# Performance work log

Measured on AMD Instinct MI355X. Metric: run time of the kernel, lower is better.

Reference implementation:

```python
import jax, jax.numpy as jnp
import numpy as np

EPS = 1e-6
THRESHOLD = 0.99
MAX_STEPS = 4
MIN_STEPS = 1
N_HEAD = 8
B, N, D, V, L, F, RCF = 1, 256, 512, 32000, 2, 1536, 2048


def rmsnorm(x, w):
    return x * jax.lax.rsqrt(jnp.mean(x * x, axis=-1, keepdims=True) + EPS) * w


def rope(x, base=10000.0):
    # x: [B, N, H, hd] -> rotary embedding (rotate-half convention)
    n, hd = x.shape[1], x.shape[-1]
    half = hd // 2
    inv = 1.0 / (base ** (jnp.arange(half, dtype=jnp.float32) * 2.0 / hd))
    ang = jnp.arange(n, dtype=jnp.float32)[:, None] * inv[None, :]  # [N, half]
    cos = jnp.cos(ang)[None, :, None, :]
    sin = jnp.sin(ang)[None, :, None, :]
    x1, x2 = x[..., :half], x[..., half:]
    return jnp.concatenate([x1 * cos - x2 * sin, x1 * sin + x2 * cos], axis=-1)


def attention(x, wqkv, wo):
    b, n, d = x.shape
    hd = d // N_HEAD
    q, k, v = jnp.split(x @ wqkv, 3, axis=-1)
    q = rope(q.reshape(b, n, N_HEAD, hd))
    k = rope(k.reshape(b, n, N_HEAD, hd))
    v = v.reshape(b, n, N_HEAD, hd)
    scores = jnp.einsum('bqhd,bkhd->bhqk', q, k) / np.float32(np.sqrt(hd))
    causal = jnp.tril(jnp.ones((n, n), dtype=bool))
    scores = jnp.where(causal, scores, jnp.float32(-1e30))
    a = jax.nn.softmax(scores, axis=-1)
    out = jnp.einsum('bhqk,bkhd->bqhd', a, v).reshape(b, n, d)
    return out @ wo


def backbone(input_ids, emb, attn_norm_w, mlp_norm_w, wqkv, wo, w_gate, w_up, w_down, final_norm_w):
    x = emb[input_ids]  # [B, N, D]
    for l in range(L):  # small fixed layer count
        x = x + attention(rmsnorm(x, attn_norm_w[l]), wqkv[l], wo[l])
        h = rmsnorm(x, mlp_norm_w[l])
        x = x + (jax.nn.silu(h @ w_gate[l]) * (h @ w_up[l])) @ w_down[l]  # SwiGLU
    return rmsnorm(x, final_norm_w)


def refinement_step(states, rc_norm_w, rc_w1, rc_w2, w_y, w_delta, w_halt, b_halt):
    h = rmsnorm(states, rc_norm_w)
    y_logits = h @ w_y                                   # [B, N, V]
    refined = states + jax.nn.gelu(h @ rc_w1) @ rc_w2    # [B, N, D]
    delta_logits = rmsnorm(refined, rc_norm_w) @ w_delta # [B, N, V]
    halt = jax.nn.sigmoid(h @ w_halt + b_halt)           # [B, N]
    combined = y_logits + delta_logits                   # compute_prediction
    return combined, halt, refined


def act_combine(halt_probs, step_logits):
    # Vectorized version of the per-(b,n) ACT halting loop.
    # halt_probs: [B, N, S]; step_logits: [B, N, S, V]
    p = halt_probs.at[..., :MIN_STEPS].set(0.0)  # min-step masking (max_steps > min_steps)
    cum = jnp.cumsum(p, axis=-1)
    prev = cum - p                      # exclusive cumulative halting prob
    running = prev < THRESHOLD          # step still executes
    is_last = jnp.arange(p.shape[-1]) == p.shape[-1] - 1
    use_rem = running & ((cum >= THRESHOLD) | is_last)  # halting step gets remainder
    weights = jnp.where(running, jnp.where(use_rem, 1.0 - prev, p), 0.0)
    final = jnp.einsum('bns,bnsv->bnv', weights, step_logits)
    remainder = jnp.sum(jnp.where(use_rem, 1.0 - prev, 0.0), axis=-1)
    ponder = jnp.sum(running, axis=-1).astype(p.dtype) + remainder  # N + R ponder cost
    return final, ponder, weights


def reference(input_ids, emb, attn_norm_w, mlp_norm_w, wqkv, wo, w_gate, w_up, w_down,
              final_norm_w, rc_norm_w, rc_w1, rc_w2, w_y, w_delta, w_halt, b_halt):
    hidden = backbone(input_ids, emb, attn_norm_w, mlp_norm_w, wqkv, wo,
                      w_gate, w_up, w_down, final_norm_w)
    states = hidden
    logits_steps, halt_steps = [], []
    for _ in range(MAX_STEPS):  # fixed refinement unroll
        combined, halt, states = refinement_step(states, rc_norm_w, rc_w1, rc_w2,
                                                 w_y, w_delta, w_halt, b_halt)
        logits_steps.append(combined)
        halt_steps.append(halt)
    step_logits = jnp.stack(logits_steps, axis=2)  # [B, N, S, V]
    halt_probs = jnp.stack(halt_steps, axis=2)     # [B, N, S]
    final_logits, ponder_costs, all_weights = act_combine(halt_probs, step_logits)
    return final_logits, ponder_costs, all_weights


def setup_inputs() -> dict:
    key = jax.random.key(0)
    ks = jax.random.split(key, 16)
    s = 0.02
    return {
        'input_ids': jax.random.randint(ks[0], (B, N), 0, V),
        'emb': jax.random.normal(ks[1], (V, D), jnp.float32) * s,
        'attn_norm_w': jnp.ones((L, D), jnp.float32),
        'mlp_norm_w': jnp.ones((L, D), jnp.float32),
        'wqkv': jax.random.normal(ks[2], (L, D, 3 * D), jnp.float32) * s,
        'wo': jax.random.normal(ks[3], (L, D, D), jnp.float32) * s,
        'w_gate': jax.random.normal(ks[4], (L, D, F), jnp.float32) * s,
        'w_up': jax.random.normal(ks[5], (L, D, F), jnp.float32) * s,
        'w_down': jax.random.normal(ks[6], (L, F, D), jnp.float32) * s,
        'final_norm_w': jnp.ones((D,), jnp.float32),
        'rc_norm_w': jnp.ones((D,), jnp.float32),
        'rc_w1': jax.random.normal(ks[7], (D, RCF), jnp.float32) * s,
        'rc_w2': jax.random.normal(ks[8], (RCF, D), jnp.float32) * s,
        'w_y': jax.random.normal(ks[9], (D, V), jnp.float32) * s,
        'w_delta': jax.random.normal(ks[10], (D, V), jnp.float32) * s,
        'w_halt': jax.random.normal(ks[11], (D,), jnp.float32) * s,
        'b_halt': jnp.zeros((), jnp.float32),
    }
```

## Files before the change

kernel.cpp:

```cpp
#include <hip/hip_runtime.h>
#include <hip/hip_bf16.h>

#define NTOK   256
#define DMODEL 512
#define NHEAD  8
#define HD     64
#define HALF   32
#define FF     1536
#define RCFF   2048
#define VOCAB  32000
#define NLAYER 2
#define NSTEPS 4
#define EPSV   1e-6f
#define THR    0.99f

typedef __attribute__((ext_vector_type(8))) short bf16x8;
typedef __attribute__((ext_vector_type(4))) float f32x4;

__global__ __launch_bounds__(256) void k_embed_norm(const int* __restrict__ ids,
                                                    const float* __restrict__ emb,
                                                    const float* __restrict__ w,
                                                    float* __restrict__ x,
                                                    float* __restrict__ xn) {
    int row = blockIdx.x, t = threadIdx.x;
    int id = ids[row];
    const float* er = emb + (size_t)id * DMODEL;
    float v0 = er[t], v1 = er[t + 256];
    float ss = v0 * v0 + v1 * v1;
    __shared__ float red[4];
    int lane = t & 63, wv = t >> 6;
    for (int o = 32; o > 0; o >>= 1) ss += __shfl_xor(ss, o);
    if (lane == 0) red[wv] = ss;
    __syncthreads();
    float tot = red[0] + red[1] + red[2] + red[3];
    float scale = rsqrtf(tot * (1.f / DMODEL) + EPSV);
    size_t base = (size_t)row * DMODEL;
    x[base + t] = v0;
    x[base + t + 256] = v1;
    xn[base + t] = v0 * scale * w[t];
    xn[base + t + 256] = v1 * scale * w[t + 256];
}

__global__ __launch_bounds__(256) void k_rmsnorm(const float* __restrict__ in,
                                                 const float* __restrict__ w,
                                                 float* __restrict__ out) {
    int row = blockIdx.x;
    const float* xr = in + (size_t)row * DMODEL;
    float s = 0.f;
    for (int d = threadIdx.x; d < DMODEL; d += 256) { float v = xr[d]; s += v * v; }
    __shared__ float red[4];
    int lane = threadIdx.x & 63, wv = threadIdx.x >> 6;
    for (int o = 32; o > 0; o >>= 1) s += __shfl_xor(s, o);
    if (lane == 0) red[wv] = s;
    __syncthreads();
    float tot = red[0] + red[1] + red[2] + red[3];
    float scale = rsqrtf(tot * (1.f / DMODEL) + EPSV);
    for (int d = threadIdx.x; d < DMODEL; d += 256)
        out[(size_t)row * DMODEL + d] = xr[d] * scale * w[d];
}

__global__ __launch_bounds__(256) void k_mm_part(const float* __restrict__ A,
                                                 const float* __restrict__ W,
                                                 float* __restrict__ Cp,
                                                 int K, int N, int kc) {
    __shared__ float As[16][68];
    __shared__ float Ws[16][68];
    const int bn = blockIdx.x * 64;
    const int bm = blockIdx.y * 64;
    const int kz = blockIdx.z * kc;
    const int tx = threadIdx.x & 15;
    const int ty = threadIdx.x >> 4;
    float ar[4], wr[4];
#pragma unroll
    for (int r = 0; r < 4; ++r) {
        int idx = threadIdx.x + r * 256;
        int m = idx >> 4, kk = idx & 15;
        ar[r] = A[(size_t)(bm + m) * K + kz + kk];
        int n = idx & 63, kw = idx >> 6;
        wr[r] = W[(size_t)(kz + kw) * N + bn + n];
    }
    float acc[4][4] = {};
    for (int k0 = kz; k0 < kz + kc; k0 += 16) {
#pragma unroll
        for (int r = 0; r < 4; ++r) {
            int idx = threadIdx.x + r * 256;
            int m = idx >> 4, kk = idx & 15;
            As[kk][m] = ar[r];
            int n = idx & 63, kw = idx >> 6;
            Ws[kw][n] = wr[r];
        }
        __syncthreads();
        if (k0 + 16 < kz + kc) {
#pragma unroll
            for (int r = 0; r < 4; ++r) {
                int idx = threadIdx.x + r * 256;
                int m = idx >> 4, kk = idx & 15;
                ar[r] = A[(size_t)(bm + m) * K + k0 + 16 + kk];
                int n = idx & 63, kw = idx >> 6;
                wr[r] = W[(size_t)(k0 + 16 + kw) * N + bn + n];
            }
        }
#pragma unroll
        for (int kk = 0; kk < 16; ++kk) {
            float4 av = *(const float4*)&As[kk][ty * 4];
            float4 bv = *(const float4*)&Ws[kk][tx * 4];
            float a[4] = {av.x, av.y, av.z, av.w};
            float b[4] = {bv.x, bv.y, bv.z, bv.w};
#pragma unroll
            for (int i = 0; i < 4; ++i)
#pragma unroll
                for (int j = 0; j < 4; ++j)
                    acc[i][j] = fmaf(a[i], b[j], acc[i][j]);
        }
        __syncthreads();
    }
    float* cp = Cp + (size_t)blockIdx.z * (size_t)(gridDim.y * 64) * N;
#pragma unroll
    for (int i = 0; i < 4; ++i) {
        int m = bm + ty * 4 + i;
#pragma unroll
        for (int j = 0; j < 4; ++j)
            cp[(size_t)m * N + bn + tx * 4 + j] = acc[i][j];
    }
}

__global__ __launch_bounds__(256) void k_gu_part(const float* __restrict__ A,
                                                 const float* __restrict__ Wg,
                                                 const float* __restrict__ Wu,
                                                 float* __restrict__ GU) {
    __shared__ float As[16][68];
    __shared__ float Ws[16][68];
    const int bn = blockIdx.x * 64;
    const int bm = blockIdx.y * 64;
    const int z = blockIdx.z;
    const float* W = (z >> 1) ? Wu : Wg;
    const int kz = (z & 1) * 256;
    const int tx = threadIdx.x & 15;
    const int ty = threadIdx.x >> 4;
    float ar[4], wr[4];
#pragma unroll
    for (int r = 0; r < 4; ++r) {
        int idx = threadIdx.x + r * 256;
        int m = idx >> 4, kk = idx & 15;
        ar[r] = A[(size_t)(bm + m) * DMODEL + kz + kk];
        int n = idx & 63, kw = idx >> 6;
        wr[r] = W[(size_t)(kz + kw) * FF + bn + n];
    }
    float acc[4][4] = {};
    for (int k0 = kz; k0 < kz + 256; k0 += 16) {
#pragma unroll
        for (int r = 0; r < 4; ++r) {
            int idx = threadIdx.x + r * 256;
            int m = idx >> 4, kk = idx & 15;
            As[kk][m] = ar[r];
            int n = idx & 63, kw = idx >> 6;
            Ws[kw][n] = wr[r];
        }
        __syncthreads();
        if (k0 + 16 < kz + 256) {
#pragma unroll
            for (int r = 0; r < 4; ++r) {
                int idx = threadIdx.x + r * 256;
                int m = idx >> 4, kk = idx & 15;
                ar[r] = A[(size_t)(bm + m) * DMODEL + k0 + 16 + kk];
                int n = idx & 63, kw = idx >> 6;
                wr[r] = W[(size_t)(k0 + 16 + kw) * FF + bn + n];
            }
        }
#pragma unroll
        for (int kk = 0; kk < 16; ++kk) {
            float4 av = *(const float4*)&As[kk][ty * 4];
            float4 bv = *(const float4*)&Ws[kk][tx * 4];
            float a[4] = {av.x, av.y, av.z, av.w};
            float b[4] = {bv.x, bv.y, bv.z, bv.w};
#pragma unroll
            for (int i = 0; i < 4; ++i)
#pragma unroll
                for (int j = 0; j < 4; ++j)
                    acc[i][j] = fmaf(a[i], b[j], acc[i][j]);
        }
        __syncthreads();
    }
    float* cp = GU + (size_t)z * (NTOK * FF);
#pragma unroll
    for (int i = 0; i < 4; ++i) {
        int m = bm + ty * 4 + i;
#pragma unroll
        for (int j = 0; j < 4; ++j)
            cp[(size_t)m * FF + bn + tx * 4 + j] = acc[i][j];
    }
}

__global__ void k_mm_finish(const float* __restrict__ Cp, const float* __restrict__ res,
                            float* __restrict__ C, int tot, int zstride, int nz, int act) {
    int i = blockIdx.x * 256 + threadIdx.x;
    if (i >= tot) return;
    float s = 0.f;
    for (int z = 0; z < nz; ++z) s += Cp[(size_t)z * zstride + i];
    if (res) s += res[i];
    if (act == 1) {
        float xg = s;
        float inner = 0.79788456080286536f * (xg + 0.044715f * xg * xg * xg);
        s = 0.5f * xg * (1.f + tanhf(inner));
    }
    C[i] = s;
}

__global__ void k_finish_silumul(const float* __restrict__ GU, float* __restrict__ C) {
    int i = blockIdx.x * 256 + threadIdx.x;
    float g = GU[i] + GU[(size_t)(NTOK * FF) + i];
    float u = GU[(size_t)(2 * NTOK * FF) + i] + GU[(size_t)(3 * NTOK * FF) + i];
    float sig = 1.f / (1.f + expf(-g));
    C[i] = g * sig * u;
}

__global__ __launch_bounds__(256) void k_finish_norm(const float* __restrict__ Cp,
                                                     const float* __restrict__ res,
                                                     const float* __restrict__ normw,
                                                     float* __restrict__ out_raw,
                                                     float* __restrict__ out_norm,
                                                     int nz) {
    int row = blockIdx.x, t = threadIdx.x;
    int c0 = t, c1 = t + 256;
    size_t base = (size_t)row * DMODEL;
    float v0 = 0.f, v1 = 0.f;
    for (int z = 0; z < nz; ++z) {
        size_t zb = (size_t)z * (NTOK * DMODEL) + base;
        v0 += Cp[zb + c0];
        v1 += Cp[zb + c1];
    }
    v0 += res[base + c0];
    v1 += res[base + c1];
    float ss = v0 * v0 + v1 * v1;
    __shared__ float red[4];
    int lane = t & 63, wv = t >> 6;
    for (int o = 32; o > 0; o >>= 1) ss += __shfl_xor(ss, o);
    if (lane == 0) red[wv] = ss;
    __syncthreads();
    float tot = red[0] + red[1] + red[2] + red[3];
    float scale = rsqrtf(tot * (1.f / DMODEL) + EPSV);
    out_raw[base + c0] = v0;
    out_raw[base + c1] = v1;
    out_norm[base + c0] = v0 * scale * normw[c0];
    out_norm[base + c1] = v1 * scale * normw[c1];
}

__global__ __launch_bounds__(256) void k_qkv_finish_rope(const float* __restrict__ Cp,
                                                         float* __restrict__ qkv) {
    int pos = blockIdx.x, t = threadIdx.x;
    int h = t >> 5, d = t & 31;
    size_t base = (size_t)pos * FF;
    auto S = [&](int col) {
        float s = 0.f;
#pragma unroll
        for (int z = 0; z < 4; ++z) s += Cp[(size_t)z * (NTOK * FF) + base + col];
        return s;
    };
    int cq0 = h * HD + d, cq1 = cq0 + HALF;
    int ck0 = DMODEL + cq0, ck1 = ck0 + HALF;
    int cv0 = 2 * DMODEL + t, cv1 = cv0 + 256;
    float q0 = S(cq0), q1 = S(cq1);
    float k0 = S(ck0), k1 = S(ck1);
    float v0 = S(cv0), v1 = S(cv1);
    float inv = powf(10000.f, -(float)d / 32.f);
    float ang = (float)pos * inv;
    float c = cosf(ang), s = sinf(ang);
    qkv[base + cq0] = q0 * c - q1 * s;
    qkv[base + cq1] = q0 * s + q1 * c;
    qkv[base + ck0] = k0 * c - k1 * s;
    qkv[base + ck1] = k0 * s + k1 * c;
    qkv[base + cv0] = v0;
    qkv[base + cv1] = v1;
}

__global__ __launch_bounds__(256) void k_attn(const float* __restrict__ qkv,
                                              float* __restrict__ out) {
    int h = blockIdx.x;
    int qi = blockIdx.y;
    int t = threadIdx.x;
    __shared__ float qs[HD];
    __shared__ float ps[NTOK];
    __shared__ float red[4];
    __shared__ float red2[4];
    __shared__ float os[4][HD];
    if (t < HD) qs[t] = qkv[(size_t)qi * FF + h * HD + t];
    __syncthreads();
    float sc = -1e30f;
    if (t <= qi) {
        const float* kr = qkv + (size_t)t * FF + DMODEL + h * HD;
        float s = 0.f;
        for (int d = 0; d < HD; ++d) s = fmaf(qs[d], kr[d], s);
        sc = s * 0.125f;
    }
    float m = sc;
    for (int o = 32; o > 0; o >>= 1) m = fmaxf(m, __shfl_xor(m, o));
    int lane = t & 63, wv = t >> 6;
    if (lane == 0) red[wv] = m;
    __syncthreads();
    m = fmaxf(fmaxf(red[0], red[1]), fmaxf(red[2], red[3]));
    float e = (t <= qi) ? expf(sc - m) : 0.f;
    ps[t] = e;
    float sum = e;
    for (int o = 32; o > 0; o >>= 1) sum += __shfl_xor(sum, o);
    if (lane == 0) red2[wv] = sum;
    __syncthreads();
    sum = red2[0] + red2[1] + red2[2] + red2[3];
    float inv = 1.f / sum;
    int d = t & 63, g = t >> 6;
    float acc = 0.f;
    for (int ki = g; ki <= qi; ki += 4)
        acc = fmaf(ps[ki], qkv[(size_t)ki * FF + 2 * DMODEL + h * HD + d], acc);
    os[g][d] = acc * inv;
    __syncthreads();
    if (t < HD)
        out[(size_t)qi * DMODEL + h * HD + t] = os[0][t] + os[1][t] + os[2][t] + os[3][t];
}

__global__ __launch_bounds__(256) void k_haltactab(const float* __restrict__ H,
                                                   const float* __restrict__ wh,
                                                   const float* __restrict__ bptr,
                                                   float* __restrict__ ponder_out,
                                                   float* __restrict__ w_out,
                                                   __hip_bfloat16* __restrict__ A,
                                                   __hip_bfloat16* __restrict__ Bm) {
    int i = blockIdx.x, t = threadIdx.x;
    int lane = t & 63, wv = t >> 6;
    __shared__ float red[4];
    __shared__ float hvals[3];
    __shared__ float hw[4];
    for (int s = 1; s <= 3; ++s) {
        const float* hr = H + ((size_t)s * NTOK + i) * DMODEL;
        float a = hr[t] * wh[t] + hr[t + 256] * wh[t + 256];
        for (int o = 32; o > 0; o >>= 1) a += __shfl_xor(a, o);
        if (lane == 0) red[wv] = a;
        __syncthreads();
        if (t == 0)
            hvals[s - 1] = 1.f / (1.f + expf(-(red[0] + red[1] + red[2] + red[3] + bptr[0])));
        __syncthreads();
    }
    if (t == 0) {
        float p[4] = {0.f, hvals[0], hvals[1], hvals[2]};
        float cum = 0.f, rem = 0.f;
        int nrun = 0;
#pragma unroll
        for (int s = 0; s < 4; ++s) {
            float prev = cum;
            cum += p[s];
            bool running = prev < THR;
            bool use_rem = running && ((cum >= THR) || (s == 3));
            float v = 0.f;
            if (running) {
                v = use_rem ? (1.f - prev) : p[s];
                if (use_rem) rem += (1.f - prev);
                nrun++;
            }
            hw[s] = v;
            w_out[i * 4 + s] = v;
        }
        ponder_out[i] = (float)nrun + rem;
    }
    __syncthreads();
    float w0 = hw[0], w1 = hw[1], w2 = hw[2], w3 = hw[3];
    size_t base = (size_t)i * DMODEL;
#pragma unroll
    for (int r = 0; r < 2; ++r) {
        int d = t + r * 256;
        float h0 = H[base + d];
        float h1 = H[(size_t)(NTOK * DMODEL) + base + d];
        float h2 = H[(size_t)(2 * NTOK * DMODEL) + base + d];
        float h3 = H[(size_t)(3 * NTOK * DMODEL) + base + d];
        float h4 = H[(size_t)(4 * NTOK * DMODEL) + base + d];
        A[base + d]  = __float2bfloat16(w0 * h0 + w1 * h1 + w2 * h2 + w3 * h3);
        Bm[base + d] = __float2bfloat16(w0 * h1 + w1 * h2 + w2 * h3 + w3 * h4);
    }
}

__global__ __launch_bounds__(512) void k_logits_mfma(const __hip_bfloat16* __restrict__ Abf,
                                                     const __hip_bfloat16* __restrict__ Bbf,
                                                     const float* __restrict__ Wy,
                                                     const float* __restrict__ Wd,
                                                     float* __restrict__ out) {
    __shared__ short Alds[256 * 32];
    __shared__ short Blds[256 * 32];
    __shared__ short Wys[32 * 70];
    __shared__ short Wds[32 * 70];
    const int tid  = threadIdx.x;
    const int wave = tid >> 6;
    const int lane = tid & 63;
    const int wrow = (wave & 1) * 128;
    const int wcol = (wave >> 1) * 16;
    const int cl   = lane & 15;
    const int kg   = lane >> 4;
    const int col  = blockIdx.x * 64 + wcol + cl;

    const int kr = tid >> 4;
    const int c4 = (tid & 15) * 4;
    const int sr0 = tid >> 2;
    const int skp = (tid & 3) * 8;

    f32x4 acc[8];
#pragma unroll
    for (int i = 0; i < 8; ++i) acc[i] = (f32x4){0.f, 0.f, 0.f, 0.f};

    const float* gy = Wy + (size_t)kr * VOCAB + blockIdx.x * 64 + c4;
    const float* gd = Wd + (size_t)kr * VOCAB + blockIdx.x * 64 + c4;

    float4 ry = *(const float4*)gy;
    float4 rd = *(const float4*)gd;
    bf16x8 ra0 = *(const bf16x8*)(Abf + (size_t)sr0 * DMODEL + skp);
    bf16x8 ra1 = *(const bf16x8*)(Abf + (size_t)(sr0 + 128) * DMODEL + skp);
    bf16x8 rb0 = *(const bf16x8*)(Bbf + (size_t)sr0 * DMODEL + skp);
    bf16x8 rb1 = *(const bf16x8*)(Bbf + (size_t)(sr0 + 128) * DMODEL + skp);

    for (int t = 0; t < 16; ++t) {
        __syncthreads();
        {
            short2 a, b;
            a.x = (short)__hip_bfloat16_raw(__float2bfloat16(ry.x)).x;
            a.y = (short)__hip_bfloat16_raw(__float2bfloat16(ry.y)).x;
            b.x = (short)__hip_bfloat16_raw(__float2bfloat16(ry.z)).x;
            b.y = (short)__hip_bfloat16_raw(__float2bfloat16(ry.w)).x;
            *(short2*)&Wys[kr * 70 + c4]     = a;
            *(short2*)&Wys[kr * 70 + c4 + 2] = b;
            a.x = (short)__hip_bfloat16_raw(__float2bfloat16(rd.x)).x;
            a.y = (short)__hip_bfloat16_raw(__float2bfloat16(rd.y)).x;
            b.x = (short)__hip_bfloat16_raw(__float2bfloat16(rd.z)).x;
            b.y = (short)__hip_bfloat16_raw(__float2bfloat16(rd.w)).x;
            *(short2*)&Wds[kr * 70 + c4]     = a;
            *(short2*)&Wds[kr * 70 + c4 + 2] = b;
            *(bf16x8*)&Alds[sr0 * 32 + skp]         = ra0;
            *(bf16x8*)&Alds[(sr0 + 128) * 32 + skp] = ra1;
            *(bf16x8*)&Blds[sr0 * 32 + skp]         = rb0;
            *(bf16x8*)&Blds[(sr0 + 128) * 32 + skp] = rb1;
        }
        if (t < 15) {
            const int kn = (t + 1) * 32;
            ry  = *(const float4*)(gy + (size_t)(t + 1) * 32 * VOCAB);
            rd  = *(const float4*)(gd + (size_t)(t + 1) * 32 * VOCAB);
            ra0 = *(const bf16x8*)(Abf + (size_t)sr0 * DMODEL + kn + skp);
            ra1 = *(const bf16x8*)(Abf + (size_t)(sr0 + 128) * DMODEL + kn + skp);
            rb0 = *(const bf16x8*)(Bbf + (size_t)sr0 * DMODEL + kn + skp);
            rb1 = *(const bf16x8*)(Bbf + (size_t)(sr0 + 128) * DMODEL + kn + skp);
        }
        __syncthreads();
        bf16x8 wy, wd;
#pragma unroll
        for (int j = 0; j < 8; ++j) {
            wy[j] = Wys[(kg * 8 + j) * 70 + wcol + cl];
            wd[j] = Wds[(kg * 8 + j) * 70 + wcol + cl];
        }
#pragma unroll
        for (int mt = 0; mt < 8; ++mt) {
            const int row = wrow + mt * 16 + cl;
            const bf16x8 a = *(const bf16x8*)&Alds[row * 32 + kg * 8];
            const bf16x8 bb = *(const bf16x8*)&Blds[row * 32 + kg * 8];
            acc[mt] = __builtin_amdgcn_mfma_f32_16x16x32_bf16(a, wy, acc[mt], 0, 0, 0);
            acc[mt] = __builtin_amdgcn_mfma_f32_16x16x32_bf16(bb, wd, acc[mt], 0, 0, 0);
        }
    }
#pragma unroll
    for (int mt = 0; mt < 8; ++mt)
#pragma unroll
        for (int r = 0; r < 4; ++r)
            out[(size_t)(wrow + mt * 16 + kg * 4 + r) * VOCAB + col] = acc[mt][r];
}

extern "C" void kernel_launch(void* const* d_in, const int* in_sizes, int n_in,
                              void* d_out, int out_size, void* d_ws, size_t ws_size,
                              hipStream_t stream) {
    const int*   ids          = (const int*)d_in[0];
    const float* emb          = (const float*)d_in[1];
    const float* attn_norm_w  = (const float*)d_in[2];
    const float* mlp_norm_w   = (const float*)d_in[3];
    const float* wqkv         = (const float*)d_in[4];
    const float* wo           = (const float*)d_in[5];
    const float* w_gate       = (const float*)d_in[6];
    const float* w_up         = (const float*)d_in[7];
    const float* w_down       = (const float*)d_in[8];
    const float* final_norm_w = (const float*)d_in[9];
    const float* rc_norm_w    = (const float*)d_in[10];
    const float* rc_w1        = (const float*)d_in[11];
    const float* rc_w2        = (const float*)d_in[12];
    const float* w_y          = (const float*)d_in[13];
    const float* w_delta      = (const float*)d_in[14];
    const float* w_halt       = (const float*)d_in[15];
    const float* b_halt       = (const float*)d_in[16];
    float* out = (float*)d_out;

    float* ws = (float*)d_ws;
    float* x       = ws + 0;
    float* xn      = ws + 131072;
    float* qkv     = ws + 262144;
    float* attnout = ws + 655360;
    float* g       = ws + 786432;
    float* t1      = ws + 1179648;
    float* states  = ws + 1703936;
    float* states2 = ws + 1835008;
    float* H       = ws + 1966080;
    __hip_bfloat16* Abf = (__hip_bfloat16*)(ws + 2623488);
    __hip_bfloat16* Bbf = (__hip_bfloat16*)(ws + 2754560);
    float* Cp      = ws + 2885632;
    float* GU      = ws + 1179648;

    k_embed_norm<<<NTOK, 256, 0, stream>>>(ids, emb, attn_norm_w, x, xn);
    for (int l = 0; l < NLAYER; ++l) {
        k_mm_part<<<dim3(FF / 64, 4, 4), 256, 0, stream>>>(
            xn, wqkv + (size_t)l * DMODEL * FF, Cp, DMODEL, FF, 128);
        k_qkv_finish_rope<<<NTOK, 256, 0, stream>>>(Cp, qkv);
        k_attn<<<dim3(NHEAD, NTOK), 256, 0, stream>>>(qkv, attnout);
        k_mm_part<<<dim3(DMODEL / 64, 4, 8), 256, 0, stream>>>(
            attnout, wo + (size_t)l * DMODEL * DMODEL, Cp, DMODEL, DMODEL, 64);
        k_finish_norm<<<NTOK, 256, 0, stream>>>(Cp, x, mlp_norm_w + l * DMODEL, x, xn, 8);
        k_gu_part<<<dim3(FF / 64, 4, 4), 256, 0, stream>>>(
            xn, w_gate + (size_t)l * DMODEL * FF, w_up + (size_t)l * DMODEL * FF, GU);
        k_finish_silumul<<<NTOK * FF / 256, 256, 0, stream>>>(GU, g);
        k_mm_part<<<dim3(DMODEL / 64, 4, 12), 256, 0, stream>>>(
            g, w_down + (size_t)l * FF * DMODEL, Cp, FF, DMODEL, 128);
        const float* nw = (l == 0) ? (attn_norm_w + DMODEL) : final_norm_w;
        float* nout = (l == 0) ? xn : states;
        k_finish_norm<<<NTOK, 256, 0, stream>>>(Cp, x, nw, x, nout, 12);
    }

    k_rmsnorm<<<NTOK, 256, 0, stream>>>(states, rc_norm_w, H);
    float* scur = states;
    float* snxt = states2;
    for (int s = 0; s < NSTEPS; ++s) {
        k_mm_part<<<dim3(RCFF / 64, 4, 4), 256, 0, stream>>>(
            H + (size_t)s * NTOK * DMODEL, rc_w1, Cp, DMODEL, RCFF, 128);
        k_mm_finish<<<NTOK * RCFF / 256, 256, 0, stream>>>(
            Cp, nullptr, t1, NTOK * RCFF, NTOK * RCFF, 4, 1);
        k_mm_part<<<dim3(DMODEL / 64, 4, 16), 256, 0, stream>>>(
            t1, rc_w2, Cp, RCFF, DMODEL, 128);
        k_finish_norm<<<NTOK, 256, 0, stream>>>(
            Cp, scur, rc_norm_w, snxt, H + (size_t)(s + 1) * NTOK * DMODEL, 16);
        float* tmp = scur; scur = snxt; snxt = tmp;
    }

    k_haltactab<<<NTOK, 256, 0, stream>>>(H, w_halt, b_halt,
                                          out + (size_t)NTOK * VOCAB,
                                          out + (size_t)NTOK * VOCAB + NTOK,
                                          Abf, Bbf);

    k_logits_mfma<<<VOCAB / 64, 512, 0, stream>>>(Abf, Bbf, w_y, w_delta, out);
}
```

Measured before the change: 374.8 us.

## Switch logits GEMM to 32x32x16 MFMA with transposed padded weight tiles

Rewrites the vocab-logits kernel to use 32x32x16 bf16 MFMA instructions. Each wave now computes a 64x32 output tile instead of 128x16. The weight tiles are stored transposed (column-major, padded to stride 40) so each lane reads its B fragment with one vector LDS load instead of eight scalar loads. The A/B LDS tiles are padded to reduce bank conflicts. The global weight loads change from float4 per thread to four strided scalar loads, which remain coalesced across the wave. The change is meant to cut LDS traffic and instruction overhead in this dominant GEMM.

```diff
diff --git a/kernel.cpp b/kernel.cpp
--- a/kernel.cpp
+++ b/kernel.cpp
@@ -16,6 +16,11 @@
 
 typedef __attribute__((ext_vector_type(8))) short bf16x8;
 typedef __attribute__((ext_vector_type(4))) float f32x4;
+typedef __attribute__((ext_vector_type(16))) float f32x16;
+
+__device__ __forceinline__ short f2b(float x) {
+    return (short)__hip_bfloat16_raw(__float2bfloat16(x)).x;
+}
 
 __global__ __launch_bounds__(256) void k_embed_norm(const int* __restrict__ ids,
                                                     const float* __restrict__ emb,
@@ -380,33 +385,36 @@
                                                      const float* __restrict__ Wy,
                                                      const float* __restrict__ Wd,
                                                      float* __restrict__ out) {
-    __shared__ short Alds[256 * 32];
-    __shared__ short Blds[256 * 32];
-    __shared__ short Wys[32 * 70];
-    __shared__ short Wds[32 * 70];
+    __shared__ short Alds[256 * 40];
+    __shared__ short Blds[256 * 40];
+    __shared__ short Wys[64 * 40];
+    __shared__ short Wds[64 * 40];
     const int tid  = threadIdx.x;
     const int wave = tid >> 6;
     const int lane = tid & 63;
-    const int wrow = (wave & 1) * 128;
-    const int wcol = (wave >> 1) * 16;
-    const int cl   = lane & 15;
-    const int kg   = lane >> 4;
-    const int col  = blockIdx.x * 64 + wcol + cl;
-
-    const int kr = tid >> 4;
-    const int c4 = (tid & 15) * 4;
+    const int l31  = lane & 31;
+    const int hi8  = (lane >> 5) * 8;
+    const int wv_row = (wave & 3) * 64;
+    const int wv_col = (wave >> 2) * 32;
+
     const int sr0 = tid >> 2;
     const int skp = (tid & 3) * 8;
-
-    f32x4 acc[8];
-#pragma unroll
-    for (int i = 0; i < 8; ++i) acc[i] = (f32x4){0.f, 0.f, 0.f, 0.f};
-
-    const float* gy = Wy + (size_t)kr * VOCAB + blockIdx.x * 64 + c4;
-    const float* gd = Wd + (size_t)kr * VOCAB + blockIdx.x * 64 + c4;
-
-    float4 ry = *(const float4*)gy;
-    float4 rd = *(const float4*)gd;
+    const int wc  = tid & 63;
+    const int wk4 = (tid >> 6) * 4;
+
+    f32x16 acc0 = {};
+    f32x16 acc1 = {};
+
+    const size_t woff = (size_t)wk4 * VOCAB + blockIdx.x * 64 + wc;
+    const float* gy = Wy + woff;
+    const float* gd = Wd + woff;
+
+    float rys[4], rds[4];
+#pragma unroll
+    for (int j = 0; j < 4; ++j) {
+        rys[j] = gy[(size_t)j * VOCAB];
+        rds[j] = gd[(size_t)j * VOCAB];
+    }
     bf16x8 ra0 = *(const bf16x8*)(Abf + (size_t)sr0 * DMODEL + skp);
     bf16x8 ra1 = *(const bf16x8*)(Abf + (size_t)(sr0 + 128) * DMODEL + skp);
     bf16x8 rb0 = *(const bf16x8*)(Bbf + (size_t)sr0 * DMODEL + skp);
@@ -415,54 +423,54 @@
     for (int t = 0; t < 16; ++t) {
         __syncthreads();
         {
-            short2 a, b;
-            a.x = (short)__hip_bfloat16_raw(__float2bfloat16(ry.x)).x;
-            a.y = (short)__hip_bfloat16_raw(__float2bfloat16(ry.y)).x;
-            b.x = (short)__hip_bfloat16_raw(__float2bfloat16(ry.z)).x;
-            b.y = (short)__hip_bfloat16_raw(__float2bfloat16(ry.w)).x;
-            *(short2*)&Wys[kr * 70 + c4]     = a;
-            *(short2*)&Wys[kr * 70 + c4 + 2] = b;
-            a.x = (short)__hip_bfloat16_raw(__float2bfloat16(rd.x)).x;
-            a.y = (short)__hip_bfloat16_raw(__float2bfloat16(rd.y)).x;
-            b.x = (short)__hip_bfloat16_raw(__float2bfloat16(rd.z)).x;
-            b.y = (short)__hip_bfloat16_raw(__float2bfloat16(rd.w)).x;
-            *(short2*)&Wds[kr * 70 + c4]     = a;
-            *(short2*)&Wds[kr * 70 + c4 + 2] = b;
-            *(bf16x8*)&Alds[sr0 * 32 + skp]         = ra0;
-            *(bf16x8*)&Alds[(sr0 + 128) * 32 + skp] = ra1;
-            *(bf16x8*)&Blds[sr0 * 32 + skp]         = rb0;
-            *(bf16x8*)&Blds[(sr0 + 128) * 32 + skp] = rb1;
+            short4 sy, sd;
+            sy.x = f2b(rys[0]); sy.y = f2b(rys[1]); sy.z = f2b(rys[2]); sy.w = f2b(rys[3]);
+            sd.x = f2b(rds[0]); sd.y = f2b(rds[1]); sd.z = f2b(rds[2]); sd.w = f2b(rds[3]);
+            *(short4*)&Wys[wc * 40 + wk4] = sy;
+            *(short4*)&Wds[wc * 40 + wk4] = sd;
+            *(bf16x8*)&Alds[sr0 * 40 + skp]         = ra0;
+            *(bf16x8*)&Alds[(sr0 + 128) * 40 + skp] = ra1;
+            *(bf16x8*)&Blds[sr0 * 40 + skp]         = rb0;
+            *(bf16x8*)&Blds[(sr0 + 128) * 40 + skp] = rb1;
         }
         if (t < 15) {
             const int kn = (t + 1) * 32;
-            ry  = *(const float4*)(gy + (size_t)(t + 1) * 32 * VOCAB);
-            rd  = *(const float4*)(gd + (size_t)(t + 1) * 32 * VOCAB);
+            const float* gy2 = gy + (size_t)kn * VOCAB;
+            const float* gd2 = gd + (size_t)kn * VOCAB;
+#pragma unroll
+            for (int j = 0; j < 4; ++j) {
+                rys[j] = gy2[(size_t)j * VOCAB];
+                rds[j] = gd2[(size_t)j * VOCAB];
+            }
             ra0 = *(const bf16x8*)(Abf + (size_t)sr0 * DMODEL + kn + skp);
             ra1 = *(const bf16x8*)(Abf + (size_t)(sr0 + 128) * DMODEL + kn + skp);
             rb0 = *(const bf16x8*)(Bbf + (size_t)sr0 * DMODEL + kn + skp);
             rb1 = *(const bf16x8*)(Bbf + (size_t)(sr0 + 128) * DMODEL + kn + skp);
         }
         __syncthreads();
-        bf16x8 wy, wd;
-#pragma unroll
-        for (int j = 0; j < 8; ++j) {
-            wy[j] = Wys[(kg * 8 + j) * 70 + wcol + cl];
-            wd[j] = Wds[(kg * 8 + j) * 70 + wcol + cl];
-        }
-#pragma unroll
-        for (int mt = 0; mt < 8; ++mt) {
-            const int row = wrow + mt * 16 + cl;
-            const bf16x8 a = *(const bf16x8*)&Alds[row * 32 + kg * 8];
-            const bf16x8 bb = *(const bf16x8*)&Blds[row * 32 + kg * 8];
-            acc[mt] = __builtin_amdgcn_mfma_f32_16x16x32_bf16(a, wy, acc[mt], 0, 0, 0);
-            acc[mt] = __builtin_amdgcn_mfma_f32_16x16x32_bf16(bb, wd, acc[mt], 0, 0, 0);
-        }
-    }
-#pragma unroll
-    for (int mt = 0; mt < 8; ++mt)
-#pragma unroll
-        for (int r = 0; r < 4; ++r)
-            out[(size_t)(wrow + mt * 16 + kg * 4 + r) * VOCAB + col] = acc[mt][r];
+#pragma unroll
+        for (int h = 0; h < 2; ++h) {
+            const int klo = h * 16 + hi8;
+            const bf16x8 wyf = *(const bf16x8*)&Wys[(wv_col + l31) * 40 + klo];
+            const bf16x8 wdf = *(const bf16x8*)&Wds[(wv_col + l31) * 40 + klo];
+            const bf16x8 ay0 = *(const bf16x8*)&Alds[(wv_row + l31) * 40 + klo];
+            const bf16x8 ay1 = *(const bf16x8*)&Alds[(wv_row + 32 + l31) * 40 + klo];
+            const bf16x8 ad0 = *(const bf16x8*)&Blds[(wv_row + l31) * 40 + klo];
+            const bf16x8 ad1 = *(const bf16x8*)&Blds[(wv_row + 32 + l31) * 40 + klo];
+            acc0 = __builtin_amdgcn_mfma_f32_32x32x16_bf16(ay0, wyf, acc0, 0, 0, 0);
+            acc0 = __builtin_amdgcn_mfma_f32_32x32x16_bf16(ad0, wdf, acc0, 0, 0, 0);
+            acc1 = __builtin_amdgcn_mfma_f32_32x32x16_bf16(ay1, wyf, acc1, 0, 0, 0);
+            acc1 = __builtin_amdgcn_mfma_f32_32x32x16_bf16(ad1, wdf, acc1, 0, 0, 0);
+        }
+    }
+    const int col = blockIdx.x * 64 + wv_col + l31;
+    const int rbase = (lane >> 5) * 4;
+#pragma unroll
+    for (int reg = 0; reg < 16; ++reg) {
+        int rowin = (reg & 3) + 8 * (reg >> 2) + rbase;
+        out[(size_t)(wv_row + rowin) * VOCAB + col] = acc0[reg];
+        out[(size_t)(wv_row + 32 + rowin) * VOCAB + col] = acc1[reg];
+    }
 }
 
 extern "C" void kernel_launch(void* const* d_in, const int* in_sizes, int n_in,
```

After: 372.2 us. No clear change (-0.7%).
